# Kernel optimization log

Measured on AMD Instinct MI355X. Metric: run time of the kernel, lower is better.

Reference implementation:

```python
import jax, jax.numpy as jnp
import numpy as np

N_NODES = 50000
N_EDGES = 1600000
IN_FEATS = 128
HIDDEN = 128
NUM_CLASSES = 40


def setup_inputs() -> dict:
    key = jax.random.key(0)
    k1, k2, k3, k4, k5 = jax.random.split(key, 5)
    features = jax.random.normal(k1, (N_NODES, IN_FEATS), dtype=jnp.float32)
    src = jax.random.randint(k2, (N_EDGES,), 0, N_NODES, dtype=jnp.int32)
    dst = jax.random.randint(k3, (N_EDGES,), 0, N_NODES, dtype=jnp.int32)
    W1 = jax.random.normal(k4, (IN_FEATS, HIDDEN), dtype=jnp.float32) / np.sqrt(IN_FEATS)
    b1 = jnp.zeros((HIDDEN,), dtype=jnp.float32)
    W2 = jax.random.normal(k5, (HIDDEN, NUM_CLASSES), dtype=jnp.float32) / np.sqrt(HIDDEN)
    b2 = jnp.zeros((NUM_CLASSES,), dtype=jnp.float32)
    return {"features": features, "src": src, "dst": dst,
            "W1": W1, "b1": b1, "W2": W2, "b2": b2}


def _degree_norms(src, dst, n_nodes):
    ones = jnp.ones(src.shape[0], dtype=jnp.float32)
    deg_out = jax.ops.segment_sum(ones, src, num_segments=n_nodes)
    deg_in = jax.ops.segment_sum(ones, dst, num_segments=n_nodes)
    # DGL GraphConv clamps degree at 1 (zero-degree nodes get norm 1)
    norm_src = jax.lax.rsqrt(jnp.maximum(deg_out, 1.0))
    norm_dst = jax.lax.rsqrt(jnp.maximum(deg_in, 1.0))
    return norm_src, norm_dst


def _graph_conv(x, W, b, src, dst, norm_src, norm_dst, n_nodes):
    # norm='both': h = D_in^{-1/2} A^T (D_out^{-1/2} x W) + b
    h = (x * norm_src[:, None]) @ W          # [N, out]
    msgs = h[src]                             # gather  [E, out]
    agg = jax.ops.segment_sum(msgs, dst, num_segments=n_nodes)  # scatter-add [N, out]
    return agg * norm_dst[:, None] + b


def reference(features, src, dst, W1, b1, W2, b2):
    n = features.shape[0]
    norm_src, norm_dst = _degree_norms(src, dst, n)
    h = jax.nn.relu(_graph_conv(features, W1, b1, src, dst, norm_src, norm_dst, n))
    h = _graph_conv(h, W2, b2, src, dst, norm_src, norm_dst, n)
    return h
```

## Files before the change

kernel.cpp:

```cpp
#include <hip/hip_runtime.h>


#define CHUNK 16384
#define CHUNK_SHIFT 14
#define NSLICES 64

__device__ __forceinline__ unsigned f2bf_bits(float f) {
    unsigned u = __float_as_uint(f);
    return (u + 0x7FFFu + ((u >> 16) & 1u)) >> 16;
}
__device__ __forceinline__ unsigned pack_bf2(float a, float b) {
    return f2bf_bits(a) | (f2bf_bits(b) << 16);
}
__device__ __forceinline__ float bflo(unsigned v) { return __uint_as_float(v << 16); }
__device__ __forceinline__ float bfhi(unsigned v) { return __uint_as_float(v & 0xFFFF0000u); }


__global__ __launch_bounds__(256) void count_kernel(const int* __restrict__ src, const int* __restrict__ dst,
                                                    unsigned int* __restrict__ part, int E, int per) {
    __shared__ unsigned int h[CHUNK];
    int c = blockIdx.y, s = blockIdx.x, t = threadIdx.x;
    #pragma unroll
    for (int i = 0; i < CHUNK / 256; ++i) h[i * 256 + t] = 0;
    __syncthreads();
    int base = c << CHUNK_SHIFT;
    int beg = s * per;
    int end = min(E, beg + per);
    int nv = (end - beg) >> 2;
    const int4* d4 = (const int4*)(dst + beg);
    const int4* s4 = (const int4*)(src + beg);
    for (int i = t; i < nv; i += 256) {
        int4 dv = d4[i];
        int4 sv = s4[i];
        int x;
        x = dv.x - base; if ((unsigned)x < CHUNK) atomicAdd(&h[x], 1u);
        x = dv.y - base; if ((unsigned)x < CHUNK) atomicAdd(&h[x], 1u);
        x = dv.z - base; if ((unsigned)x < CHUNK) atomicAdd(&h[x], 1u);
        x = dv.w - base; if ((unsigned)x < CHUNK) atomicAdd(&h[x], 1u);
        x = sv.x - base; if ((unsigned)x < CHUNK) atomicAdd(&h[x], 0x10000u);
        x = sv.y - base; if ((unsigned)x < CHUNK) atomicAdd(&h[x], 0x10000u);
        x = sv.z - base; if ((unsigned)x < CHUNK) atomicAdd(&h[x], 0x10000u);
        x = sv.w - base; if ((unsigned)x < CHUNK) atomicAdd(&h[x], 0x10000u);
    }
    for (int e = beg + (nv << 2) + t; e < end; e += 256) {
        int x = dst[e] - base; if ((unsigned)x < CHUNK) atomicAdd(&h[x], 1u);
        x = src[e] - base;     if ((unsigned)x < CHUNK) atomicAdd(&h[x], 0x10000u);
    }
    __syncthreads();
    unsigned int* out = part + (((size_t)(c * NSLICES + s)) << CHUNK_SHIFT);
    #pragma unroll
    for (int i = 0; i < CHUNK / 256; ++i) out[i * 256 + t] = h[i * 256 + t];
}

__global__ __launch_bounds__(256) void reduce_kernel(const unsigned int* __restrict__ part,
                                                     float* __restrict__ norm_src, float* __restrict__ norm_dst,
                                                     int* __restrict__ deg_dst_i, int N) {
    int d = blockIdx.x * 256 + threadIdx.x;
    if (d >= N) return;
    int c = d >> CHUNK_SHIFT, idx = d & (CHUNK - 1);
    const unsigned int* p = part + (((size_t)c * NSLICES) << CHUNK_SHIFT) + idx;
    unsigned int dsum = 0, ssum = 0;
    #pragma unroll
    for (int s = 0; s < NSLICES; ++s) {
        unsigned int v = p[(size_t)s << CHUNK_SHIFT];
        dsum += v & 0xFFFFu;
        ssum += v >> 16;
    }
    deg_dst_i[d] = (int)dsum;
    norm_src[d] = rsqrtf(fmaxf((float)ssum, 1.0f));
    norm_dst[d] = rsqrtf(fmaxf((float)dsum, 1.0f));
}

__global__ __launch_bounds__(256) void scanA_kernel(const int* __restrict__ deg, int* __restrict__ bsum, int N) {
    __shared__ int wsum[4];
    int b = blockIdx.x, t = threadIdx.x, lane = t & 63, wid = t >> 6;
    int i0 = b * 1024 + t * 4;
    int s = 0;
    if (i0 + 3 < N) {
        int4 v = *(const int4*)(deg + i0);
        s = v.x + v.y + v.z + v.w;
    } else {
        for (int k = 0; k < 4; ++k) { int i = i0 + k; if (i < N) s += deg[i]; }
    }
    #pragma unroll
    for (int off = 32; off; off >>= 1) s += __shfl_down(s, off, 64);
    if (lane == 0) wsum[wid] = s;
    __syncthreads();
    if (t == 0) bsum[b] = wsum[0] + wsum[1] + wsum[2] + wsum[3];
}

__global__ __launch_bounds__(64) void scanB_kernel(int* __restrict__ bsum, int NB,
                                                   int* __restrict__ row_ptr, int N) {
    int t = threadIdx.x;
    int v = (t < NB) ? bsum[t] : 0;
    int x = v;
    #pragma unroll
    for (int off = 1; off < 64; off <<= 1) {
        int y = __shfl_up(x, off, 64);
        if (t >= off) x += y;
    }
    if (t < NB) bsum[t] = x - v;
    if (t == 63) row_ptr[N] = x;
}

__global__ __launch_bounds__(256) void scanC_kernel(const int* __restrict__ deg, const int* __restrict__ bsum,
                                                    int* __restrict__ row_ptr, int N) {
    __shared__ int wsum[4];
    int b = blockIdx.x, t = threadIdx.x, lane = t & 63, wid = t >> 6;
    int i0 = b * 1024 + t * 4;
    int4 v = make_int4(0, 0, 0, 0);
    if (i0 + 3 < N) v = *(const int4*)(deg + i0);
    else {
        v.x = (i0 < N) ? deg[i0] : 0;
        v.y = (i0 + 1 < N) ? deg[i0 + 1] : 0;
        v.z = (i0 + 2 < N) ? deg[i0 + 2] : 0;
        v.w = (i0 + 3 < N) ? deg[i0 + 3] : 0;
    }
    int tsum = v.x + v.y + v.z + v.w;
    int x = tsum;
    #pragma unroll
    for (int off = 1; off < 64; off <<= 1) {
        int y = __shfl_up(x, off, 64);
        if (lane >= off) x += y;
    }
    if (lane == 63) wsum[wid] = x;
    __syncthreads();
    int woff = 0;
    for (int k = 0; k < wid; ++k) woff += wsum[k];
    int base = bsum[b] + woff + (x - tsum);
    int e0 = base, e1 = e0 + v.x, e2 = e1 + v.y, e3 = e2 + v.z;
    if (i0 + 3 < N) *(int4*)(row_ptr + i0) = make_int4(e0, e1, e2, e3);
    else {
        if (i0 < N) row_ptr[i0] = e0;
        if (i0 + 1 < N) row_ptr[i0 + 1] = e1;
        if (i0 + 2 < N) row_ptr[i0 + 2] = e2;
        if (i0 + 3 < N) row_ptr[i0 + 3] = e3;
    }
}

__global__ __launch_bounds__(256) void offsets_kernel(unsigned int* __restrict__ part,
                                                      const int* __restrict__ row_ptr, int N) {
    int d = blockIdx.x * 256 + threadIdx.x;
    if (d >= N) return;
    int c = d >> CHUNK_SHIFT, idx = d & (CHUNK - 1);
    unsigned int* p = part + (((size_t)c * NSLICES) << CHUNK_SHIFT) + idx;
    unsigned int running = (unsigned int)row_ptr[d];
    #pragma unroll
    for (int s = 0; s < NSLICES; ++s) {
        unsigned int v = p[(size_t)s << CHUNK_SHIFT];
        p[(size_t)s << CHUNK_SHIFT] = running;
        running += v & 0xFFFFu;
    }
}

__global__ __launch_bounds__(256) void scatter_kernel(const int* __restrict__ src, const int* __restrict__ dst,
                                                      const unsigned int* __restrict__ cum,
                                                      int* __restrict__ col, int E, int per) {
    __shared__ int cur[CHUNK];
    int c = blockIdx.y, s = blockIdx.x, t = threadIdx.x;
    const unsigned int* cc = cum + (((size_t)(c * NSLICES + s)) << CHUNK_SHIFT);
    #pragma unroll
    for (int i = 0; i < CHUNK / 256; ++i) cur[i * 256 + t] = (int)cc[i * 256 + t];
    __syncthreads();
    int base = c << CHUNK_SHIFT;
    int beg = s * per;
    int end = min(E, beg + per);
    int nv = (end - beg) >> 2;
    const int4* d4 = (const int4*)(dst + beg);
    const int4* s4 = (const int4*)(src + beg);
    for (int i = t; i < nv; i += 256) {
        int4 dv = d4[i];
        int4 sv = s4[i];
        int x;
        x = dv.x - base; if ((unsigned)x < CHUNK) col[atomicAdd(&cur[x], 1)] = sv.x;
        x = dv.y - base; if ((unsigned)x < CHUNK) col[atomicAdd(&cur[x], 1)] = sv.y;
        x = dv.z - base; if ((unsigned)x < CHUNK) col[atomicAdd(&cur[x], 1)] = sv.z;
        x = dv.w - base; if ((unsigned)x < CHUNK) col[atomicAdd(&cur[x], 1)] = sv.w;
    }
    for (int e = beg + (nv << 2) + t; e < end; e += 256) {
        int x = dst[e] - base;
        if ((unsigned)x < CHUNK) col[atomicAdd(&cur[x], 1)] = src[e];
    }
}


__global__ __launch_bounds__(256) void gemm1_kernel(const float* __restrict__ x, const float* __restrict__ norm,
                                                    const float* __restrict__ W, unsigned short* __restrict__ h1u,
                                                    int N) {
    __shared__ float xs[128 * 32];
    __shared__ float ws[128 * 64];
    int t = threadIdx.x;
    int rb = blockIdx.x * 32;
    int jb = blockIdx.y * 64;
    #pragma unroll
    for (int i = 0; i < 8; ++i) {
        int idx = i * 256 + t;
        int k = idx >> 4, j4 = (idx & 15) << 2;
        *(float4*)(ws + k * 64 + j4) = *(const float4*)(W + k * 128 + jb + j4);
    }
    #pragma unroll
    for (int i = 0; i < 4; ++i) {
        int idx = i * 256 + t;
        int row = idx >> 5, m = idx & 31, k4 = m << 2;
        int gr = rb + row;
        float4 v = make_float4(0.f, 0.f, 0.f, 0.f);
        if (gr < N) {
            v = *(const float4*)(x + (size_t)gr * 128 + k4);
            float nm = norm[gr];
            v.x *= nm; v.y *= nm; v.z *= nm; v.w *= nm;
        }
        int r = row ^ ((m & 7) << 2);
        xs[(k4 + 0) * 32 + r] = v.x;
        xs[(k4 + 1) * 32 + r] = v.y;
        xs[(k4 + 2) * 32 + r] = v.z;
        xs[(k4 + 3) * 32 + r] = v.w;
    }
    __syncthreads();
    int jg = t & 15, rg = t >> 4;
    int j = jg << 2, r0 = rg << 1;
    float a00 = 0, a01 = 0, a02 = 0, a03 = 0;
    float a10 = 0, a11 = 0, a12 = 0, a13 = 0;
    #pragma unroll 8
    for (int k = 0; k < 128; ++k) {
        int sw = ((k >> 2) & 7) << 2;
        float2 xv = *(const float2*)&xs[k * 32 + (r0 ^ sw)];
        float4 wv = *(const float4*)&ws[k * 64 + j];
        a00 += xv.x * wv.x; a01 += xv.x * wv.y; a02 += xv.x * wv.z; a03 += xv.x * wv.w;
        a10 += xv.y * wv.x; a11 += xv.y * wv.y; a12 += xv.y * wv.z; a13 += xv.y * wv.w;
    }
    int gr0 = rb + r0;
    if (gr0 < N) {
        uint2 p = make_uint2(pack_bf2(a00, a01), pack_bf2(a02, a03));
        *(uint2*)(h1u + (size_t)gr0 * 128 + jb + j) = p;
    }
    if (gr0 + 1 < N) {
        uint2 p = make_uint2(pack_bf2(a10, a11), pack_bf2(a12, a13));
        *(uint2*)(h1u + (size_t)(gr0 + 1) * 128 + jb + j) = p;
    }
}

__global__ __launch_bounds__(256) void agg1_kernel(const int* __restrict__ row_ptr, const int* __restrict__ col,
                                                   const unsigned int* __restrict__ h1p, const float* __restrict__ norm_dst,
                                                   const float* __restrict__ b1, unsigned int* __restrict__ x2p, int N) {
    int n = (blockIdx.x * 256 + threadIdx.x) >> 6;
    int lane = threadIdx.x & 63;
    if (n >= N) return;
    int beg = row_ptr[n], end = row_ptr[n + 1];
    float ax = 0.f, ay = 0.f;
    int e = beg;
    for (; e + 4 <= end; e += 4) {
        int s0 = col[e], s1 = col[e + 1], s2 = col[e + 2], s3 = col[e + 3];
        unsigned v0 = h1p[(size_t)s0 * 64 + lane];
        unsigned v1 = h1p[(size_t)s1 * 64 + lane];
        unsigned v2 = h1p[(size_t)s2 * 64 + lane];
        unsigned v3 = h1p[(size_t)s3 * 64 + lane];
        ax += bflo(v0); ay += bfhi(v0);
        ax += bflo(v1); ay += bfhi(v1);
        ax += bflo(v2); ay += bfhi(v2);
        ax += bflo(v3); ay += bfhi(v3);
    }
    for (; e < end; ++e) {
        unsigned v = h1p[(size_t)col[e] * 64 + lane];
        ax += bflo(v); ay += bfhi(v);
    }
    float nd = norm_dst[n];
    float2 b = ((const float2*)b1)[lane];
    float ox = fmaxf(ax * nd + b.x, 0.f);
    float oy = fmaxf(ay * nd + b.y, 0.f);
    x2p[(size_t)n * 64 + lane] = pack_bf2(ox, oy);
}

__global__ __launch_bounds__(256) void gemm2_kernel(const unsigned int* __restrict__ x2p, const float* __restrict__ norm,
                                                    const float* __restrict__ W, unsigned short* __restrict__ h2u, int N) {
    __shared__ float xs[128 * 64];
    __shared__ float ws2[128 * 40];
    int t = threadIdx.x;
    int rb = blockIdx.x * 64;
    #pragma unroll
    for (int i = 0; i < 5; ++i) {
        int idx = i * 256 + t;
        *(float4*)(ws2 + idx * 4) = *(const float4*)(W + idx * 4);
    }
    #pragma unroll
    for (int i = 0; i < 16; ++i) {
        int idx = i * 256 + t;
        int row = idx >> 6, kp = idx & 63;
        int gr = rb + row;
        unsigned v = 0; float nm = 0.f;
        if (gr < N) {
            v = x2p[(size_t)gr * 64 + kp];
            nm = norm[gr];
        }
        int r = row ^ (((kp >> 1) & 7) << 2);
        xs[(2 * kp + 0) * 64 + r] = bflo(v) * nm;
        xs[(2 * kp + 1) * 64 + r] = bfhi(v) * nm;
    }
    __syncthreads();
    int jg = t & 7, rg = t >> 3;
    int j = jg * 5, r0 = rg << 1;
    float acc0[5] = {0, 0, 0, 0, 0};
    float acc1[5] = {0, 0, 0, 0, 0};
    #pragma unroll 4
    for (int k = 0; k < 128; ++k) {
        int sw = ((k >> 2) & 7) << 2;
        float2 xv = *(const float2*)&xs[k * 64 + (r0 ^ sw)];
        #pragma unroll
        for (int c = 0; c < 5; ++c) {
            float w = ws2[k * 40 + j + c];
            acc0[c] += xv.x * w;
            acc1[c] += xv.y * w;
        }
    }
    int gr0 = rb + r0;
    if (gr0 < N) {
        #pragma unroll
        for (int c = 0; c < 5; ++c) h2u[(size_t)gr0 * 40 + j + c] = (unsigned short)f2bf_bits(acc0[c]);
    }
    if (gr0 + 1 < N) {
        #pragma unroll
        for (int c = 0; c < 5; ++c) h2u[(size_t)(gr0 + 1) * 40 + j + c] = (unsigned short)f2bf_bits(acc1[c]);
    }
}

__global__ __launch_bounds__(256) void agg2_kernel(const int* __restrict__ row_ptr, const int* __restrict__ col,
                                                   const unsigned short* __restrict__ h2u, const float* __restrict__ norm_dst,
                                                   const float* __restrict__ b2, float* __restrict__ out, int N) {
    int n = (blockIdx.x * 256 + threadIdx.x) >> 6;
    int lane = threadIdx.x & 63;
    if (n >= N) return;
    int beg = row_ptr[n], end = row_ptr[n + 1];
    float acc = 0.f;
    bool act = lane < 40;
    int e = beg;
    for (; e + 4 <= end; e += 4) {
        int s0 = col[e], s1 = col[e + 1], s2 = col[e + 2], s3 = col[e + 3];
        if (act) {
            acc += __uint_as_float((unsigned)h2u[(size_t)s0 * 40 + lane] << 16);
            acc += __uint_as_float((unsigned)h2u[(size_t)s1 * 40 + lane] << 16);
            acc += __uint_as_float((unsigned)h2u[(size_t)s2 * 40 + lane] << 16);
            acc += __uint_as_float((unsigned)h2u[(size_t)s3 * 40 + lane] << 16);
        }
    }
    for (; e < end; ++e) {
        int s = col[e];
        if (act) acc += __uint_as_float((unsigned)h2u[(size_t)s * 40 + lane] << 16);
    }
    if (act) out[(size_t)n * 40 + lane] = acc * norm_dst[n] + b2[lane];
}

extern "C" void kernel_launch(void* const* d_in, const int* in_sizes, int n_in,
                              void* d_out, int out_size, void* d_ws, size_t ws_size,
                              hipStream_t stream) {
    const float* x  = (const float*)d_in[0];
    const int* src  = (const int*)d_in[1];
    const int* dst  = (const int*)d_in[2];
    const float* W1 = (const float*)d_in[3];
    const float* b1 = (const float*)d_in[4];
    const float* W2 = (const float*)d_in[5];
    const float* b2 = (const float*)d_in[6];
    float* out = (float*)d_out;

    int N = in_sizes[0] / 128;
    int E = in_sizes[1];
    int NPAD = (N + 63) & ~63;
    int NCHUNKS = (N + CHUNK - 1) >> CHUNK_SHIFT;
    int per = ((E + NSLICES - 1) / NSLICES + 3) & ~3;
    int NB = (N + 1023) / 1024;

    float* ws = (float*)d_ws;
    float* norm_src = ws;
    float* norm_dst = ws + NPAD;
    int* deg_dst_i  = (int*)(ws + 2 * (size_t)NPAD);
    int* row_ptr    = (int*)(ws + 3 * (size_t)NPAD);
    int* bsum       = (int*)(ws + 4 * (size_t)NPAD);
    int* col        = (int*)(ws + 4 * (size_t)NPAD + 64);
    size_t h1_off   = ((size_t)4 * NPAD + 64 + E + 15) & ~(size_t)15;
    unsigned short* h1u = (unsigned short*)(ws + h1_off);
    unsigned int*   h1p = (unsigned int*)h1u;
    unsigned int*   x2p = h1p + (size_t)NPAD * 64;
    unsigned short* h2u = h1u;
    unsigned int*   part = (unsigned int*)h1u;

    dim3 cgrid(NSLICES, NCHUNKS);
    count_kernel<<<cgrid, 256, 0, stream>>>(src, dst, part, E, per);
    reduce_kernel<<<(N + 255) / 256, 256, 0, stream>>>(part, norm_src, norm_dst, deg_dst_i, N);
    scanA_kernel<<<NB, 256, 0, stream>>>(deg_dst_i, bsum, N);
    scanB_kernel<<<1, 64, 0, stream>>>(bsum, NB, row_ptr, N);
    scanC_kernel<<<NB, 256, 0, stream>>>(deg_dst_i, bsum, row_ptr, N);
    offsets_kernel<<<(N + 255) / 256, 256, 0, stream>>>(part, row_ptr, N);
    scatter_kernel<<<cgrid, 256, 0, stream>>>(src, dst, part, col, E, per);
    gemm1_kernel<<<dim3((N + 31) / 32, 2), 256, 0, stream>>>(x, norm_src, W1, h1u, N);
    agg1_kernel<<<(N * 64 + 255) / 256, 256, 0, stream>>>(row_ptr, col, h1p, norm_dst, b1, x2p, N);
    gemm2_kernel<<<(N + 63) / 64, 256, 0, stream>>>(x2p, norm_src, W2, h2u, N);
    agg2_kernel<<<(N * 64 + 255) / 256, 256, 0, stream>>>(row_ptr, col, h2u, norm_dst, b2, out, N);
}
```

Before: 239.2 us.

## Tile hidden features into XCD-local column slabs and add nontemporal hints

The first-layer hidden matrix is stored as four 32-column bf16 slabs, each laid out node-major. The agg1 grid maps block ids so that each pair of XCDs handles one slab, which shrinks the gather working set per XCD's L2. Each wavefront now aggregates four nodes with 16 lanes each, and gemm1 and gemm2 are adapted to the new layout. Nontemporal loads and stores are added to streaming accesses (edge lists, partial histograms, col) to reduce cache pollution. The cost is more column-index reloads per edge and divergence when the four nodes in a wave have different degrees.

```diff
diff --git a/kernel.cpp b/kernel.cpp
--- a/kernel.cpp
+++ b/kernel.cpp
@@ -4,6 +4,9 @@
 #define CHUNK 16384
 #define CHUNK_SHIFT 14
 #define NSLICES 64
+#define TQ 16
+
+typedef int iv4 __attribute__((ext_vector_type(4)));
 
 __device__ __forceinline__ unsigned f2bf_bits(float f) {
     unsigned u = __float_as_uint(f);
@@ -27,11 +30,11 @@
     int beg = s * per;
     int end = min(E, beg + per);
     int nv = (end - beg) >> 2;
-    const int4* d4 = (const int4*)(dst + beg);
-    const int4* s4 = (const int4*)(src + beg);
+    const iv4* d4 = (const iv4*)(dst + beg);
+    const iv4* s4 = (const iv4*)(src + beg);
     for (int i = t; i < nv; i += 256) {
-        int4 dv = d4[i];
-        int4 sv = s4[i];
+        iv4 dv = __builtin_nontemporal_load(d4 + i);
+        iv4 sv = __builtin_nontemporal_load(s4 + i);
         int x;
         x = dv.x - base; if ((unsigned)x < CHUNK) atomicAdd(&h[x], 1u);
         x = dv.y - base; if ((unsigned)x < CHUNK) atomicAdd(&h[x], 1u);
@@ -49,7 +52,7 @@
     __syncthreads();
     unsigned int* out = part + (((size_t)(c * NSLICES + s)) << CHUNK_SHIFT);
     #pragma unroll
-    for (int i = 0; i < CHUNK / 256; ++i) out[i * 256 + t] = h[i * 256 + t];
+    for (int i = 0; i < CHUNK / 256; ++i) __builtin_nontemporal_store(h[i * 256 + t], out + i * 256 + t);
 }
 
 __global__ __launch_bounds__(256) void reduce_kernel(const unsigned int* __restrict__ part,
@@ -62,7 +65,7 @@
     unsigned int dsum = 0, ssum = 0;
     #pragma unroll
     for (int s = 0; s < NSLICES; ++s) {
-        unsigned int v = p[(size_t)s << CHUNK_SHIFT];
+        unsigned int v = __builtin_nontemporal_load(p + ((size_t)s << CHUNK_SHIFT));
         dsum += v & 0xFFFFu;
         ssum += v >> 16;
     }
@@ -147,8 +150,8 @@
     unsigned int running = (unsigned int)row_ptr[d];
     #pragma unroll
     for (int s = 0; s < NSLICES; ++s) {
-        unsigned int v = p[(size_t)s << CHUNK_SHIFT];
-        p[(size_t)s << CHUNK_SHIFT] = running;
+        unsigned int v = __builtin_nontemporal_load(p + ((size_t)s << CHUNK_SHIFT));
+        __builtin_nontemporal_store(running, p + ((size_t)s << CHUNK_SHIFT));
         running += v & 0xFFFFu;
     }
 }
@@ -160,17 +163,17 @@
     int c = blockIdx.y, s = blockIdx.x, t = threadIdx.x;
     const unsigned int* cc = cum + (((size_t)(c * NSLICES + s)) << CHUNK_SHIFT);
     #pragma unroll
-    for (int i = 0; i < CHUNK / 256; ++i) cur[i * 256 + t] = (int)cc[i * 256 + t];
+    for (int i = 0; i < CHUNK / 256; ++i) cur[i * 256 + t] = (int)__builtin_nontemporal_load(cc + i * 256 + t);
     __syncthreads();
     int base = c << CHUNK_SHIFT;
     int beg = s * per;
     int end = min(E, beg + per);
     int nv = (end - beg) >> 2;
-    const int4* d4 = (const int4*)(dst + beg);
-    const int4* s4 = (const int4*)(src + beg);
+    const iv4* d4 = (const iv4*)(dst + beg);
+    const iv4* s4 = (const iv4*)(src + beg);
     for (int i = t; i < nv; i += 256) {
-        int4 dv = d4[i];
-        int4 sv = s4[i];
+        iv4 dv = __builtin_nontemporal_load(d4 + i);
+        iv4 sv = __builtin_nontemporal_load(s4 + i);
         int x;
         x = dv.x - base; if ((unsigned)x < CHUNK) col[atomicAdd(&cur[x], 1)] = sv.x;
         x = dv.y - base; if ((unsigned)x < CHUNK) col[atomicAdd(&cur[x], 1)] = sv.y;
@@ -185,8 +188,8 @@
 
 
 __global__ __launch_bounds__(256) void gemm1_kernel(const float* __restrict__ x, const float* __restrict__ norm,
-                                                    const float* __restrict__ W, unsigned short* __restrict__ h1u,
-                                                    int N) {
+                                                    const float* __restrict__ W, unsigned int* __restrict__ h1t,
+                                                    int N, int NPAD) {
     __shared__ float xs[128 * 32];
     __shared__ float ws[128 * 64];
     int t = threadIdx.x;
@@ -228,50 +231,72 @@
         a00 += xv.x * wv.x; a01 += xv.x * wv.y; a02 += xv.x * wv.z; a03 += xv.x * wv.w;
         a10 += xv.y * wv.x; a11 += xv.y * wv.y; a12 += xv.y * wv.z; a13 += xv.y * wv.w;
     }
+    int c0 = jb + j;
+    int tile = c0 >> 5;
+    int uo = (c0 & 31) >> 1;
+    unsigned int* base = h1t + (size_t)tile * NPAD * TQ + uo;
     int gr0 = rb + r0;
-    if (gr0 < N) {
-        uint2 p = make_uint2(pack_bf2(a00, a01), pack_bf2(a02, a03));
-        *(uint2*)(h1u + (size_t)gr0 * 128 + jb + j) = p;
-    }
-    if (gr0 + 1 < N) {
-        uint2 p = make_uint2(pack_bf2(a10, a11), pack_bf2(a12, a13));
-        *(uint2*)(h1u + (size_t)(gr0 + 1) * 128 + jb + j) = p;
-    }
+    if (gr0 < N)     *(uint2*)(base + (size_t)gr0 * TQ)       = make_uint2(pack_bf2(a00, a01), pack_bf2(a02, a03));
+    if (gr0 + 1 < N) *(uint2*)(base + (size_t)(gr0 + 1) * TQ) = make_uint2(pack_bf2(a10, a11), pack_bf2(a12, a13));
 }
 
 __global__ __launch_bounds__(256) void agg1_kernel(const int* __restrict__ row_ptr, const int* __restrict__ col,
-                                                   const unsigned int* __restrict__ h1p, const float* __restrict__ norm_dst,
-                                                   const float* __restrict__ b1, unsigned int* __restrict__ x2p, int N) {
-    int n = (blockIdx.x * 256 + threadIdx.x) >> 6;
-    int lane = threadIdx.x & 63;
-    if (n >= N) return;
-    int beg = row_ptr[n], end = row_ptr[n + 1];
+                                                   const unsigned int* __restrict__ h1t, const float* __restrict__ norm_dst,
+                                                   const float* __restrict__ b1, unsigned int* __restrict__ x2t,
+                                                   int N, int NPAD, int Bt) {
+    int bid = blockIdx.x;
+    int xcd = bid & 7;
+    int tile = xcd >> 1;
+    int nblk = (bid >> 3) * 2 + (xcd & 1);
+    if (nblk >= Bt) return;
+    int t = threadIdx.x;
+    int wid = t >> 6, lane = t & 63;
+    int g = lane >> 4, f = lane & 15;
+    int nb = nblk * 16 + wid * 4 + g;
+    int beg = 0, deg = 0;
+    if (nb < N) { beg = row_ptr[nb]; deg = row_ptr[nb + 1] - beg; }
+    int md = deg;
+    md = max(md, __shfl_xor(md, 16, 64));
+    md = max(md, __shfl_xor(md, 32, 64));
+    const unsigned int* hb = h1t + (size_t)tile * NPAD * TQ + f;
+    const int* cp = col + beg;
     float ax = 0.f, ay = 0.f;
-    int e = beg;
-    for (; e + 4 <= end; e += 4) {
-        int s0 = col[e], s1 = col[e + 1], s2 = col[e + 2], s3 = col[e + 3];
-        unsigned v0 = h1p[(size_t)s0 * 64 + lane];
-        unsigned v1 = h1p[(size_t)s1 * 64 + lane];
-        unsigned v2 = h1p[(size_t)s2 * 64 + lane];
-        unsigned v3 = h1p[(size_t)s3 * 64 + lane];
-        ax += bflo(v0); ay += bfhi(v0);
-        ax += bflo(v1); ay += bfhi(v1);
-        ax += bflo(v2); ay += bfhi(v2);
-        ax += bflo(v3); ay += bfhi(v3);
-    }
-    for (; e < end; ++e) {
-        unsigned v = h1p[(size_t)col[e] * 64 + lane];
-        ax += bflo(v); ay += bfhi(v);
-    }
-    float nd = norm_dst[n];
-    float2 b = ((const float2*)b1)[lane];
-    float ox = fmaxf(ax * nd + b.x, 0.f);
-    float oy = fmaxf(ay * nd + b.y, 0.f);
-    x2p[(size_t)n * 64 + lane] = pack_bf2(ox, oy);
-}
-
-__global__ __launch_bounds__(256) void gemm2_kernel(const unsigned int* __restrict__ x2p, const float* __restrict__ norm,
-                                                    const float* __restrict__ W, unsigned short* __restrict__ h2u, int N) {
+    for (int e = 0; e < md; e += 4) {
+        int r = deg - e;
+        if (r > 0) {
+            int s0 = __builtin_nontemporal_load(cp + e);
+            unsigned v = hb[(size_t)s0 * TQ];
+            ax += bflo(v); ay += bfhi(v);
+        }
+        if (r > 1) {
+            int s1 = __builtin_nontemporal_load(cp + e + 1);
+            unsigned v = hb[(size_t)s1 * TQ];
+            ax += bflo(v); ay += bfhi(v);
+        }
+        if (r > 2) {
+            int s2 = __builtin_nontemporal_load(cp + e + 2);
+            unsigned v = hb[(size_t)s2 * TQ];
+            ax += bflo(v); ay += bfhi(v);
+        }
+        if (r > 3) {
+            int s3 = __builtin_nontemporal_load(cp + e + 3);
+            unsigned v = hb[(size_t)s3 * TQ];
+            ax += bflo(v); ay += bfhi(v);
+        }
+    }
+    if (nb < N) {
+        float nd = norm_dst[nb];
+        float2 b = ((const float2*)b1)[tile * TQ + f];
+        float ox = fmaxf(ax * nd + b.x, 0.f);
+        float oy = fmaxf(ay * nd + b.y, 0.f);
+        __builtin_nontemporal_store(pack_bf2(ox, oy),
+                                    x2t + (size_t)tile * NPAD * TQ + (size_t)nb * TQ + f);
+    }
+}
+
+__global__ __launch_bounds__(256) void gemm2_kernel(const unsigned int* __restrict__ x2t, const float* __restrict__ norm,
+                                                    const float* __restrict__ W, unsigned short* __restrict__ h2u,
+                                                    int N, int NPAD) {
     __shared__ float xs[128 * 64];
     __shared__ float ws2[128 * 40];
     int t = threadIdx.x;
@@ -288,7 +313,7 @@
         int gr = rb + row;
         unsigned v = 0; float nm = 0.f;
         if (gr < N) {
-            v = x2p[(size_t)gr * 64 + kp];
+            v = x2t[(size_t)(kp >> 4) * NPAD * TQ + (size_t)gr * TQ + (kp & 15)];
             nm = norm[gr];
         }
         int r = row ^ (((kp >> 1) & 7) << 2);
@@ -333,7 +358,10 @@
     bool act = lane < 40;
     int e = beg;
     for (; e + 4 <= end; e += 4) {
-        int s0 = col[e], s1 = col[e + 1], s2 = col[e + 2], s3 = col[e + 3];
+        int s0 = __builtin_nontemporal_load(col + e);
+        int s1 = __builtin_nontemporal_load(col + e + 1);
+        int s2 = __builtin_nontemporal_load(col + e + 2);
+        int s3 = __builtin_nontemporal_load(col + e + 3);
         if (act) {
             acc += __uint_as_float((unsigned)h2u[(size_t)s0 * 40 + lane] << 16);
             acc += __uint_as_float((unsigned)h2u[(size_t)s1 * 40 + lane] << 16);
@@ -342,7 +370,7 @@
         }
     }
     for (; e < end; ++e) {
-        int s = col[e];
+        int s = __builtin_nontemporal_load(col + e);
         if (act) acc += __uint_as_float((unsigned)h2u[(size_t)s * 40 + lane] << 16);
     }
     if (act) out[(size_t)n * 40 + lane] = acc * norm_dst[n] + b2[lane];
@@ -375,11 +403,10 @@
     int* bsum       = (int*)(ws + 4 * (size_t)NPAD);
     int* col        = (int*)(ws + 4 * (size_t)NPAD + 64);
     size_t h1_off   = ((size_t)4 * NPAD + 64 + E + 15) & ~(size_t)15;
-    unsigned short* h1u = (unsigned short*)(ws + h1_off);
-    unsigned int*   h1p = (unsigned int*)h1u;
-    unsigned int*   x2p = h1p + (size_t)NPAD * 64;
-    unsigned short* h2u = h1u;
-    unsigned int*   part = (unsigned int*)h1u;
+    unsigned int* h1t = (unsigned int*)(ws + h1_off);
+    unsigned int* x2t = h1t + (size_t)NPAD * 64;
+    unsigned short* h2u = (unsigned short*)h1t;
+    unsigned int* part = h1t;
 
     dim3 cgrid(NSLICES, NCHUNKS);
     count_kernel<<<cgrid, 256, 0, stream>>>(src, dst, part, E, per);
@@ -389,8 +416,10 @@
     scanC_kernel<<<NB, 256, 0, stream>>>(deg_dst_i, bsum, row_ptr, N);
     offsets_kernel<<<(N + 255) / 256, 256, 0, stream>>>(part, row_ptr, N);
     scatter_kernel<<<cgrid, 256, 0, stream>>>(src, dst, part, col, E, per);
-    gemm1_kernel<<<dim3((N + 31) / 32, 2), 256, 0, stream>>>(x, norm_src, W1, h1u, N);
-    agg1_kernel<<<(N * 64 + 255) / 256, 256, 0, stream>>>(row_ptr, col, h1p, norm_dst, b1, x2p, N);
-    gemm2_kernel<<<(N + 63) / 64, 256, 0, stream>>>(x2p, norm_src, W2, h2u, N);
+    gemm1_kernel<<<dim3((N + 31) / 32, 2), 256, 0, stream>>>(x, norm_src, W1, h1t, N, NPAD);
+    int Bt = (N + 15) / 16;
+    int P = (Bt + 1) / 2;
+    agg1_kernel<<<8 * P, 256, 0, stream>>>(row_ptr, col, h1t, norm_dst, b1, x2t, N, NPAD, Bt);
+    gemm2_kernel<<<(N + 63) / 64, 256, 0, stream>>>(x2t, norm_src, W2, h2u, N, NPAD);
     agg2_kernel<<<(N * 64 + 255) / 256, 256, 0, stream>>>(row_ptr, col, h2u, norm_dst, b2, out, N);
 }
```

Result: slower. 408.0 us (+70.6%).
